# Kernel optimization log

Hardware: AMD Instinct MI355X
Metric: run time of the kernel (lower is better)

The kernel has to match this reference:

```python
import jax, jax.numpy as jnp
import numpy as np

N_HEADS = 16
N_KV_HEADS = 4
N_EMBED = 2048
HEAD_DIM = 128
SECTIONS = [16, 24, 24, 16, 24, 24]


def _process_rotary(c):
    # c: [3, B, T, HEAD_DIM] -> [B, 1, T, HEAD_DIM]
    splits = np.cumsum(SECTIONS)[:-1]
    secs = jnp.split(c, splits, axis=-1)
    out = jnp.concatenate([s[i % 3] for i, s in enumerate(secs)], axis=-1)
    return out[:, None]  # add head axis


def _rotate_half(x):
    x1, x2 = jnp.split(x, 2, axis=-1)
    return jnp.concatenate([-x2, x1], axis=-1)


def setup_inputs() -> dict:
    key = jax.random.key(0)
    ks = jax.random.split(key, 12)
    B, T = 1, 2048
    s = 0.02
    return {
        "x": jax.random.normal(ks[0], (B, T, N_EMBED), jnp.float32),
        "cos": jax.random.uniform(ks[1], (3, B, T, HEAD_DIM), jnp.float32),
        "sin": jax.random.uniform(ks[2], (3, B, T, HEAD_DIM), jnp.float32),
        "Wq": jax.random.normal(ks[3], (N_EMBED, N_EMBED), jnp.float32) * s,
        "bq": jax.random.normal(ks[4], (N_EMBED,), jnp.float32) * s,
        "Wk": jax.random.normal(ks[5], (N_EMBED, N_KV_HEADS * HEAD_DIM), jnp.float32) * s,
        "bk": jax.random.normal(ks[6], (N_KV_HEADS * HEAD_DIM,), jnp.float32) * s,
        "Wv": jax.random.normal(ks[7], (N_EMBED, N_KV_HEADS * HEAD_DIM), jnp.float32) * s,
        "bv": jax.random.normal(ks[8], (N_KV_HEADS * HEAD_DIM,), jnp.float32) * s,
        "Wo": jax.random.normal(ks[9], (N_EMBED, N_EMBED), jnp.float32) * s,
    }


def reference(x, cos, sin, Wq, bq, Wk, bk, Wv, bv, Wo):
    B, T, C = x.shape
    H, Hkv, D = N_HEADS, N_KV_HEADS, HEAD_DIM
    q = (x @ Wq + bq).reshape(B, T, H, D).transpose(0, 2, 1, 3)    # [B,H,T,D]
    k = (x @ Wk + bk).reshape(B, T, Hkv, D).transpose(0, 2, 1, 3)  # [B,Hkv,T,D]
    v = (x @ Wv + bv).reshape(B, T, Hkv, D).transpose(0, 2, 1, 3)
    # multi-section rope (cos/sin are 4-dim -> custom path)
    c = _process_rotary(cos)
    s = _process_rotary(sin)
    q = q * c + _rotate_half(q) * s
    k = k * c + _rotate_half(k) * s
    present_k, present_v = k, v
    # GQA expansion (repeat_interleave over head axis)
    r = H // Hkv
    k = jnp.repeat(k, r, axis=1)
    v = jnp.repeat(v, r, axis=1)
    # causal SDPA
    scores = jnp.einsum("bhqd,bhkd->bhqk", q, k) / jnp.sqrt(jnp.float32(D))
    causal = jnp.tril(jnp.ones((T, T), dtype=bool))
    scores = jnp.where(causal, scores, jnp.finfo(scores.dtype).min)
    attn = jax.nn.softmax(scores, axis=-1)
    y = jnp.einsum("bhqk,bhkd->bhqd", attn, v)
    y = y.transpose(0, 2, 1, 3).reshape(B, T, C)
    y = y @ Wo
    return (y, present_k, present_v)
```

## Files before the change

kernel.cpp:

```cpp
#include <hip/hip_runtime.h>

typedef unsigned short u16;
typedef __attribute__((ext_vector_type(4))) float f32x4;
typedef __attribute__((ext_vector_type(8))) __bf16 bf16x8;
typedef __attribute__((ext_vector_type(4))) u16 u16x4;


__device__ __forceinline__ u16 f2bf(float f) {
  union { float f; unsigned u; } v; v.f = f;
  unsigned r = v.u + 0x7fffu + ((v.u >> 16) & 1u);
  return (u16)(r >> 16);
}

__device__ __forceinline__ void stage16(const void* g, void* l) {
#if __has_builtin(__builtin_amdgcn_global_load_lds)
  __builtin_amdgcn_global_load_lds((const __attribute__((address_space(1))) void*)g,
                                   (__attribute__((address_space(3))) void*)l, 16, 0, 0);
#else
  *(f32x4*)l = *(const f32x4*)g;
#endif
}

__device__ __forceinline__ f32x4 mfma16(bf16x8 a, bf16x8 b, f32x4 c) {
  return __builtin_amdgcn_mfma_f32_16x16x32_bf16(a, b, c, 0, 0, 0);
}

__device__ __forceinline__ float fexp2(float x) {
#if __has_builtin(__builtin_amdgcn_exp2f)
  return __builtin_amdgcn_exp2f(x);
#else
  return exp2f(x);
#endif
}

__device__ __forceinline__ int rope_ch(int d) {
  int dd = (d < 64) ? d : d - 64;
  return (dd < 16) ? 0 : (dd < 40 ? 1 : 2);
}


__global__ void yuna_convert_bf16(const float* __restrict__ in, u16* __restrict__ out, int n4) {
  int i = blockIdx.x * blockDim.x + threadIdx.x;
  if (i < n4) {
    f32x4 v = ((const f32x4*)in)[i];
    u16x4 o;
    o.x = f2bf(v.x); o.y = f2bf(v.y); o.z = f2bf(v.z); o.w = f2bf(v.w);
    ((u16x4*)out)[i] = o;
  }
}

__global__ void yuna_transpose_bf16(const float* __restrict__ W, u16* __restrict__ out, int N) {
  __shared__ float tile[64][65];
  int k0 = blockIdx.x * 64, n0 = blockIdx.y * 64;
  int tx = threadIdx.x & 63, ty = threadIdx.x >> 6;
#pragma unroll
  for (int j = 0; j < 64; j += 4)
    tile[ty + j][tx] = W[(size_t)(k0 + ty + j) * N + n0 + tx];
  __syncthreads();
#pragma unroll
  for (int j = 0; j < 64; j += 4)
    out[(size_t)(n0 + ty + j) * 2048 + k0 + tx] = f2bf(tile[tx][ty + j]);
}

__global__ void yuna_transpose_v(const float* __restrict__ pv, u16* __restrict__ vtb) {
  __shared__ float tile[64][65];
  int t0 = blockIdx.x * 64, d0 = blockIdx.y * 64, kvh = blockIdx.z;
  int tx = threadIdx.x & 63, ty = threadIdx.x >> 6;
#pragma unroll
  for (int j = 0; j < 64; j += 4)
    tile[ty + j][tx] = pv[(size_t)(kvh * 2048 + t0 + ty + j) * 128 + d0 + tx];
  __syncthreads();
#pragma unroll
  for (int j = 0; j < 64; j += 4)
    vtb[(size_t)(kvh * 128 + d0 + ty + j) * 2048 + t0 + tx] = f2bf(tile[tx][ty + j]);
}

template <int WN>
__global__ __launch_bounds__(256, 2) void yuna_gemm_bt(
    const u16* __restrict__ A, const u16* __restrict__ Bt,
    float* __restrict__ C, int M, int N, int K) {
  constexpr int NF = WN / 16;
  constexpr int BROWS = 2 * WN;
  __shared__ __align__(16) u16 As[128 * 64];
  __shared__ __align__(16) u16 Bs[BROWS * 64];
  const int tid = threadIdx.x;
  const int wave = tid >> 6, lane = tid & 63;
  const int m0 = blockIdx.x * 128, n0 = blockIdx.y * (2 * WN);
  const int wr = (wave >> 1) * 64, wc = (wave & 1) * WN;
  const int lrow = lane & 15, lkg = lane >> 4;

  const int srow = tid >> 3;
  const int ssc = (tid & 7) ^ ((tid >> 3) & 7);
  const size_t abase = (size_t)(m0 + srow) * K + ssc * 8;
  const size_t bbase = (size_t)(n0 + srow) * K + ssc * 8;

  const f32x4 fzero = {0.f, 0.f, 0.f, 0.f};
  f32x4 acc[4][NF];
#pragma unroll
  for (int mi = 0; mi < 4; ++mi)
#pragma unroll
    for (int ni = 0; ni < NF; ++ni) acc[mi][ni] = fzero;

  const int sw = lrow & 7;
  for (int k0 = 0; k0 < K; k0 += 64) {
    __syncthreads();
#pragma unroll
    for (int it = 0; it < 4; ++it)
      stage16(A + abase + (size_t)it * 32 * K + k0, (char*)As + (tid + it * 256) * 16);
#pragma unroll
    for (int it = 0; it < BROWS / 32; ++it)
      stage16(Bt + bbase + (size_t)it * 32 * K + k0, (char*)Bs + (tid + it * 256) * 16);
    asm volatile("s_waitcnt vmcnt(0)" ::: "memory");
    __syncthreads();
#pragma unroll
    for (int kk = 0; kk < 2; ++kk) {
      const int cof = ((kk * 4 + lkg) ^ sw) << 4;
      bf16x8 af[4], bfr[NF];
#pragma unroll
      for (int mi = 0; mi < 4; ++mi)
        af[mi] = *(const bf16x8*)((const char*)As + (wr + mi * 16 + lrow) * 128 + cof);
#pragma unroll
      for (int ni = 0; ni < NF; ++ni)
        bfr[ni] = *(const bf16x8*)((const char*)Bs + (wc + ni * 16 + lrow) * 128 + cof);
#pragma unroll
      for (int mi = 0; mi < 4; ++mi)
#pragma unroll
        for (int ni = 0; ni < NF; ++ni)
          acc[mi][ni] = mfma16(af[mi], bfr[ni], acc[mi][ni]);
    }
  }
#pragma unroll
  for (int mi = 0; mi < 4; ++mi)
#pragma unroll
    for (int ni = 0; ni < NF; ++ni) {
      int r0 = m0 + wr + mi * 16 + lkg * 4;
      int c = n0 + wc + ni * 16 + lrow;
#pragma unroll
      for (int r = 0; r < 4; ++r)
        C[(size_t)(r0 + r) * N + c] = acc[mi][ni][r];
    }
}

__global__ void yuna_rope_scatter(
    const float* __restrict__ qkv, const float* __restrict__ bq,
    const float* __restrict__ bk, const float* __restrict__ bv,
    const float* __restrict__ cosp, const float* __restrict__ sinp,
    u16* __restrict__ qb, u16* __restrict__ kb,
    float* __restrict__ pk, float* __restrict__ pv) {
  const float QSCALE = 1.4426950408889634f * 0.08838834764831845f;
  int t = blockIdx.x;
  int tid = threadIdx.x;
  const float* row = qkv + (size_t)t * 3072;
  size_t cbase = (size_t)t * 128;
  for (int i = tid; i < 1024; i += 256) {
    int h = i >> 6, d = i & 63;
    float a = row[h * 128 + d] + bq[h * 128 + d];
    float b = row[h * 128 + d + 64] + bq[h * 128 + d + 64];
    float c0 = cosp[(size_t)rope_ch(d) * 262144 + cbase + d];
    float s0 = sinp[(size_t)rope_ch(d) * 262144 + cbase + d];
    float c1 = cosp[(size_t)rope_ch(d + 64) * 262144 + cbase + d + 64];
    float s1 = sinp[(size_t)rope_ch(d + 64) * 262144 + cbase + d + 64];
    float o0 = a * c0 - b * s0;
    float o1 = b * c1 + a * s1;
    size_t o = ((size_t)h * 2048 + t) * 128 + d;
    qb[o] = f2bf(o0 * QSCALE);
    qb[o + 64] = f2bf(o1 * QSCALE);
  }
  {
    int kvh = tid >> 6, d = tid & 63;
    float a = row[2048 + kvh * 128 + d] + bk[kvh * 128 + d];
    float b = row[2048 + kvh * 128 + d + 64] + bk[kvh * 128 + d + 64];
    float c0 = cosp[(size_t)rope_ch(d) * 262144 + cbase + d];
    float s0 = sinp[(size_t)rope_ch(d) * 262144 + cbase + d];
    float c1 = cosp[(size_t)rope_ch(d + 64) * 262144 + cbase + d + 64];
    float s1 = sinp[(size_t)rope_ch(d + 64) * 262144 + cbase + d + 64];
    float o0 = a * c0 - b * s0;
    float o1 = b * c1 + a * s1;
    size_t o = ((size_t)kvh * 2048 + t) * 128 + d;
    kb[o] = f2bf(o0); kb[o + 64] = f2bf(o1);
    pk[o] = o0; pk[o + 64] = o1;
  }
  for (int i = tid; i < 512; i += 256) {
    int kvh = i >> 7, d = i & 127;
    pv[((size_t)kvh * 2048 + t) * 128 + d] = row[2560 + kvh * 128 + d] + bv[kvh * 128 + d];
  }
}

__global__ __launch_bounds__(128, 2) void yuna_flash_attn(
    const u16* __restrict__ Q,
    const u16* __restrict__ Kb,
    const u16* __restrict__ Vt,
    u16* __restrict__ Y) {
  __shared__ __align__(16) u16 Ks[64 * 128];
  __shared__ __align__(16) u16 Vs[128 * 64];
  const int h = blockIdx.x;
  const int yb = blockIdx.y;
  const int qb = (yb & 1) ? (31 - (yb >> 1)) : (yb >> 1);
  const int kvh = h >> 2;
  const int tid = threadIdx.x, wave = tid >> 6, lane = tid & 63;
  const int lrow = lane & 15, lkg = lane >> 4;
  const int mloc0 = wave * 32;
  const int sw = lrow & 7;

  const int krow = tid >> 4;
  const int ksc = (tid & 15) ^ ((tid >> 4) & 7);
  const size_t kbase0 = ((size_t)(kvh * 2048 + krow) << 7) + ksc * 8;
  const int vrow = tid >> 3;
  const int vsc = (tid & 7) ^ ((tid >> 3) & 7);
  const size_t vbase0 = (size_t)(kvh * 128 + vrow) * 2048 + vsc * 8;

  bf16x8 qf[2][4];
#pragma unroll
  for (int mt = 0; mt < 2; ++mt)
#pragma unroll
    for (int kk = 0; kk < 4; ++kk)
      qf[mt][kk] = *(const bf16x8*)(Q + (((size_t)h * 2048 + qb * 64 + mloc0 + mt * 16 + lrow) << 7) + kk * 32 + lkg * 8);

  const f32x4 fzero = {0.f, 0.f, 0.f, 0.f};
  f32x4 o[8][2];
#pragma unroll
  for (int dt = 0; dt < 8; ++dt) { o[dt][0] = fzero; o[dt][1] = fzero; }
  float m_i[2] = {-1e30f, -1e30f}, l_i[2] = {0.f, 0.f};

  const int nkb = qb + 1;
  for (int kb = 0; kb < nkb; ++kb) {
    __syncthreads();
#pragma unroll
    for (int it = 0; it < 8; ++it)
      stage16(Kb + kbase0 + ((size_t)(kb * 64 + it * 8) << 7), (char*)Ks + (tid + it * 128) * 16);
#pragma unroll
    for (int it = 0; it < 8; ++it)
      stage16(Vt + vbase0 + (size_t)it * 16 * 2048 + kb * 64, (char*)Vs + (tid + it * 128) * 16);
    asm volatile("s_waitcnt vmcnt(0)" ::: "memory");
    __syncthreads();

    f32x4 s[4][2];
#pragma unroll
    for (int nt = 0; nt < 4; ++nt) { s[nt][0] = fzero; s[nt][1] = fzero; }
#pragma unroll
    for (int kk = 0; kk < 4; ++kk) {
      const int cof = ((kk * 4 + lkg) ^ sw) << 4;
      bf16x8 kf[4];
#pragma unroll
      for (int nt = 0; nt < 4; ++nt)
        kf[nt] = *(const bf16x8*)((const char*)Ks + (nt * 16 + lrow) * 256 + cof);
#pragma unroll
      for (int nt = 0; nt < 4; ++nt)
#pragma unroll
        for (int mt = 0; mt < 2; ++mt)
          s[nt][mt] = mfma16(kf[nt], qf[mt][kk], s[nt][mt]);
    }
    if (kb == qb) {
#pragma unroll
      for (int nt = 0; nt < 4; ++nt)
#pragma unroll
        for (int mt = 0; mt < 2; ++mt) {
          int m = mloc0 + mt * 16 + lrow;
#pragma unroll
          for (int r = 0; r < 4; ++r)
            if (nt * 16 + lkg * 4 + r > m) s[nt][mt][r] = -1e30f;
        }
    }
    __syncthreads();

    float alpha[2];
#pragma unroll
    for (int mt = 0; mt < 2; ++mt) {
      float mx = -1e30f;
#pragma unroll
      for (int nt = 0; nt < 4; ++nt)
#pragma unroll
        for (int r = 0; r < 4; ++r) mx = fmaxf(mx, s[nt][mt][r]);
      mx = fmaxf(mx, __shfl_xor(mx, 16));
      mx = fmaxf(mx, __shfl_xor(mx, 32));
      float mnew = fmaxf(m_i[mt], mx);
      alpha[mt] = fexp2(m_i[mt] - mnew);
      m_i[mt] = mnew;
      float ps = 0.f;
      const int m = mloc0 + mt * 16 + lrow;
      const int hh = lkg & 1;
#pragma unroll
      for (int nt = 0; nt < 4; ++nt) {
        u16x4 p4;
#pragma unroll
        for (int r = 0; r < 4; ++r) {
          float p = fexp2(s[nt][mt][r] - mnew);
          ps += p;
          p4[r] = f2bf(p);
        }
        int cc = 2 * nt + (lkg >> 1);
        *(u16x4*)((char*)Ks + m * 128 + ((cc ^ (m & 7)) << 4) + hh * 8) = p4;
      }
      ps += __shfl_xor(ps, 16);
      ps += __shfl_xor(ps, 32);
      l_i[mt] = l_i[mt] * alpha[mt] + ps;
    }
#pragma unroll
    for (int dt = 0; dt < 8; ++dt) {
      o[dt][0] *= alpha[0];
      o[dt][1] *= alpha[1];
    }

#pragma unroll
    for (int kk = 0; kk < 2; ++kk) {
      const int cof = ((kk * 4 + lkg) ^ sw) << 4;
      bf16x8 pf[2], vf[8];
#pragma unroll
      for (int mt = 0; mt < 2; ++mt) {
        int m = mloc0 + mt * 16 + lrow;
        pf[mt] = *(const bf16x8*)((const char*)Ks + m * 128 + cof);
      }
#pragma unroll
      for (int dt = 0; dt < 8; ++dt)
        vf[dt] = *(const bf16x8*)((const char*)Vs + (dt * 16 + lrow) * 128 + cof);
#pragma unroll
      for (int dt = 0; dt < 8; ++dt)
#pragma unroll
        for (int mt = 0; mt < 2; ++mt)
          o[dt][mt] = mfma16(vf[dt], pf[mt], o[dt][mt]);
    }
  }

  __syncthreads();
#pragma unroll
  for (int mt = 0; mt < 2; ++mt) {
    float inv = 1.f / l_i[mt];
    int m = mloc0 + mt * 16 + lrow;
    const int hh = lkg & 1;
#pragma unroll
    for (int dt = 0; dt < 8; ++dt) {
      u16x4 w4;
#pragma unroll
      for (int r = 0; r < 4; ++r) w4[r] = f2bf(o[dt][mt][r] * inv);
      int cc = 2 * dt + (lkg >> 1);
      *(u16x4*)((char*)Ks + m * 256 + ((cc ^ (m & 7)) << 4) + hh * 8) = w4;
    }
  }
  __syncthreads();
#pragma unroll
  for (int it = 0; it < 8; ++it) {
    int c = tid + it * 128;
    int row = c >> 4, cc = c & 15;
    f32x4 v = *(const f32x4*)((const char*)Ks + row * 256 + ((cc ^ (row & 7)) << 4));
    *(f32x4*)(Y + (size_t)(qb * 64 + row) * 2048 + h * 128 + cc * 8) = v;
  }
}


extern "C" void kernel_launch(void* const* d_in, const int* in_sizes, int n_in,
                              void* d_out, int out_size, void* d_ws, size_t ws_size,
                              hipStream_t stream) {
  const float* x = (const float*)d_in[0];
  const float* cosp = (const float*)d_in[1];
  const float* sinp = (const float*)d_in[2];
  const float* Wq = (const float*)d_in[3];
  const float* bq = (const float*)d_in[4];
  const float* Wk = (const float*)d_in[5];
  const float* bk = (const float*)d_in[6];
  const float* Wv = (const float*)d_in[7];
  const float* bv = (const float*)d_in[8];
  const float* Wo = (const float*)d_in[9];
  float* out = (float*)d_out;
  float* out_k = out + 4194304;
  float* out_v = out + 5242880;

  char* ws = (char*)d_ws;
  u16* xb   = (u16*)(ws + 0);
  u16* Wb   = (u16*)(ws + 8388608);
  u16* Wob  = (u16*)(ws + 20971520);
  float* qkv = (float*)(ws + 29360128);
  u16* qbuf = (u16*)(ws + 54525952);
  u16* kbuf = (u16*)(ws + 62914560);
  u16* vtb  = (u16*)(ws + 65011712);
  u16* yat  = (u16*)(ws + 67108864);

  yuna_convert_bf16<<<4096, 256, 0, stream>>>(x, xb, 1048576);
  yuna_transpose_bf16<<<dim3(32, 32), 256, 0, stream>>>(Wq, Wb, 2048);
  yuna_transpose_bf16<<<dim3(32, 8), 256, 0, stream>>>(Wk, Wb + (size_t)2048 * 2048, 512);
  yuna_transpose_bf16<<<dim3(32, 8), 256, 0, stream>>>(Wv, Wb + (size_t)2560 * 2048, 512);
  yuna_transpose_bf16<<<dim3(32, 32), 256, 0, stream>>>(Wo, Wob, 2048);
  yuna_gemm_bt<48><<<dim3(16, 32), 256, 0, stream>>>(xb, Wb, qkv, 2048, 3072, 2048);
  yuna_rope_scatter<<<2048, 256, 0, stream>>>(qkv, bq, bk, bv, cosp, sinp,
                                              qbuf, kbuf, out_k, out_v);
  yuna_transpose_v<<<dim3(32, 2, 4), 256, 0, stream>>>(out_v, vtb);
  yuna_flash_attn<<<dim3(16, 32), 128, 0, stream>>>(qbuf, kbuf, vtb, yat);
  yuna_gemm_bt<32><<<dim3(16, 32), 256, 0, stream>>>(yat, Wob, out, 2048, 2048, 2048);
}
```

Before: 270.4 us.

## Double-buffer K/V tiles in flash attention and merge weight transposes into one launch

The flash attention kernel now keeps two LDS buffers for K and V and prefetches the next key block while computing on the current one, waiting with partial vmcnt counts and raw s_barrier. P gets its own LDS buffer so it no longer overwrites K. The query-block ordering across blockIdx.y is changed, and the four weight transpose launches are fused into one 3D-grid launch with early exit for the smaller matrices. The larger LDS footprint may lower occupancy, and the ordering of the hand-written waitcnt and barrier calls has to be correct.

```diff
diff --git a/kernel.cpp b/kernel.cpp
--- a/kernel.cpp
+++ b/kernel.cpp
@@ -49,9 +49,20 @@
   }
 }
 
-__global__ void yuna_transpose_bf16(const float* __restrict__ W, u16* __restrict__ out, int N) {
+__global__ void yuna_prep_weights(const float* __restrict__ Wq, const float* __restrict__ Wk,
+                                  const float* __restrict__ Wv, const float* __restrict__ Wo,
+                                  u16* __restrict__ Wb, u16* __restrict__ Wob) {
   __shared__ float tile[64][65];
+  const int mat = blockIdx.z;
+  const float* W;
+  u16* out;
+  int N;
+  if (mat == 0)      { W = Wq; out = Wb;                          N = 2048; }
+  else if (mat == 1) { W = Wk; out = Wb + (size_t)2048 * 2048;    N = 512; }
+  else if (mat == 2) { W = Wv; out = Wb + (size_t)2560 * 2048;    N = 512; }
+  else               { W = Wo; out = Wob;                         N = 2048; }
   int k0 = blockIdx.x * 64, n0 = blockIdx.y * 64;
+  if (n0 >= N) return;
   int tx = threadIdx.x & 63, ty = threadIdx.x >> 6;
 #pragma unroll
   for (int j = 0; j < 64; j += 4)
@@ -191,11 +202,12 @@
     const u16* __restrict__ Kb,
     const u16* __restrict__ Vt,
     u16* __restrict__ Y) {
-  __shared__ __align__(16) u16 Ks[64 * 128];
-  __shared__ __align__(16) u16 Vs[128 * 64];
+  __shared__ __align__(16) u16 Ks[2][64 * 128];
+  __shared__ __align__(16) u16 Vs[2][128 * 64];
+  __shared__ __align__(16) u16 Ps[64 * 64];
   const int h = blockIdx.x;
   const int yb = blockIdx.y;
-  const int qb = (yb & 1) ? (31 - (yb >> 1)) : (yb >> 1);
+  const int qb = (yb < 16) ? yb : 47 - yb;
   const int kvh = h >> 2;
   const int tid = threadIdx.x, wave = tid >> 6, lane = tid & 63;
   const int lrow = lane & 15, lkg = lane >> 4;
@@ -223,16 +235,31 @@
   float m_i[2] = {-1e30f, -1e30f}, l_i[2] = {0.f, 0.f};
 
   const int nkb = qb + 1;
+
+#pragma unroll
+  for (int it = 0; it < 8; ++it)
+    stage16(Kb + kbase0 + ((size_t)(it * 8) << 7), (char*)Ks[0] + (tid + it * 128) * 16);
+#pragma unroll
+  for (int it = 0; it < 8; ++it)
+    stage16(Vt + vbase0 + (size_t)it * 16 * 2048, (char*)Vs[0] + (tid + it * 128) * 16);
+
   for (int kb = 0; kb < nkb; ++kb) {
-    __syncthreads();
-#pragma unroll
-    for (int it = 0; it < 8; ++it)
-      stage16(Kb + kbase0 + ((size_t)(kb * 64 + it * 8) << 7), (char*)Ks + (tid + it * 128) * 16);
-#pragma unroll
-    for (int it = 0; it < 8; ++it)
-      stage16(Vt + vbase0 + (size_t)it * 16 * 2048 + kb * 64, (char*)Vs + (tid + it * 128) * 16);
-    asm volatile("s_waitcnt vmcnt(0)" ::: "memory");
-    __syncthreads();
+    const int cur = kb & 1;
+    const char* Ksb = (const char*)Ks[cur];
+    const char* Vsb = (const char*)Vs[cur];
+    if (kb + 1 < nkb) {
+      char* Ksn = (char*)Ks[cur ^ 1];
+      char* Vsn = (char*)Vs[cur ^ 1];
+#pragma unroll
+      for (int it = 0; it < 8; ++it)
+        stage16(Kb + kbase0 + ((size_t)((kb + 1) * 64 + it * 8) << 7), Ksn + (tid + it * 128) * 16);
+#pragma unroll
+      for (int it = 0; it < 8; ++it)
+        stage16(Vt + vbase0 + (size_t)it * 16 * 2048 + (kb + 1) * 64, Vsn + (tid + it * 128) * 16);
+      asm volatile("s_waitcnt vmcnt(16)\n\ts_barrier" ::: "memory");
+    } else {
+      asm volatile("s_waitcnt vmcnt(0)\n\ts_barrier" ::: "memory");
+    }
 
     f32x4 s[4][2];
 #pragma unroll
@@ -243,7 +270,7 @@
       bf16x8 kf[4];
 #pragma unroll
       for (int nt = 0; nt < 4; ++nt)
-        kf[nt] = *(const bf16x8*)((const char*)Ks + (nt * 16 + lrow) * 256 + cof);
+        kf[nt] = *(const bf16x8*)(Ksb + (nt * 16 + lrow) * 256 + cof);
 #pragma unroll
       for (int nt = 0; nt < 4; ++nt)
 #pragma unroll
@@ -261,7 +288,6 @@
             if (nt * 16 + lkg * 4 + r > m) s[nt][mt][r] = -1e30f;
         }
     }
-    __syncthreads();
 
     float alpha[2];
 #pragma unroll
@@ -289,7 +315,7 @@
           p4[r] = f2bf(p);
         }
         int cc = 2 * nt + (lkg >> 1);
-        *(u16x4*)((char*)Ks + m * 128 + ((cc ^ (m & 7)) << 4) + hh * 8) = p4;
+        *(u16x4*)((char*)Ps + m * 128 + ((cc ^ (m & 7)) << 4) + hh * 8) = p4;
       }
       ps += __shfl_xor(ps, 16);
       ps += __shfl_xor(ps, 32);
@@ -308,17 +334,18 @@
 #pragma unroll
       for (int mt = 0; mt < 2; ++mt) {
         int m = mloc0 + mt * 16 + lrow;
-        pf[mt] = *(const bf16x8*)((const char*)Ks + m * 128 + cof);
+        pf[mt] = *(const bf16x8*)((char*)Ps + m * 128 + cof);
       }
 #pragma unroll
       for (int dt = 0; dt < 8; ++dt)
-        vf[dt] = *(const bf16x8*)((const char*)Vs + (dt * 16 + lrow) * 128 + cof);
+        vf[dt] = *(const bf16x8*)(Vsb + (dt * 16 + lrow) * 128 + cof);
 #pragma unroll
       for (int dt = 0; dt < 8; ++dt)
 #pragma unroll
         for (int mt = 0; mt < 2; ++mt)
           o[dt][mt] = mfma16(vf[dt], pf[mt], o[dt][mt]);
     }
+    asm volatile("s_barrier" ::: "memory");
   }
 
   __syncthreads();
@@ -333,7 +360,7 @@
 #pragma unroll
       for (int r = 0; r < 4; ++r) w4[r] = f2bf(o[dt][mt][r] * inv);
       int cc = 2 * dt + (lkg >> 1);
-      *(u16x4*)((char*)Ks + m * 256 + ((cc ^ (m & 7)) << 4) + hh * 8) = w4;
+      *(u16x4*)((char*)Ks[0] + m * 256 + ((cc ^ (m & 7)) << 4) + hh * 8) = w4;
     }
   }
   __syncthreads();
@@ -341,7 +368,7 @@
   for (int it = 0; it < 8; ++it) {
     int c = tid + it * 128;
     int row = c >> 4, cc = c & 15;
-    f32x4 v = *(const f32x4*)((const char*)Ks + row * 256 + ((cc ^ (row & 7)) << 4));
+    f32x4 v = *(const f32x4*)((const char*)Ks[0] + row * 256 + ((cc ^ (row & 7)) << 4));
     *(f32x4*)(Y + (size_t)(qb * 64 + row) * 2048 + h * 128 + cc * 8) = v;
   }
 }
@@ -375,10 +402,7 @@
   u16* yat  = (u16*)(ws + 67108864);
 
   yuna_convert_bf16<<<4096, 256, 0, stream>>>(x, xb, 1048576);
-  yuna_transpose_bf16<<<dim3(32, 32), 256, 0, stream>>>(Wq, Wb, 2048);
-  yuna_transpose_bf16<<<dim3(32, 8), 256, 0, stream>>>(Wk, Wb + (size_t)2048 * 2048, 512);
-  yuna_transpose_bf16<<<dim3(32, 8), 256, 0, stream>>>(Wv, Wb + (size_t)2560 * 2048, 512);
-  yuna_transpose_bf16<<<dim3(32, 32), 256, 0, stream>>>(Wo, Wob, 2048);
+  yuna_prep_weights<<<dim3(32, 32, 4), 256, 0, stream>>>(Wq, Wk, Wv, Wo, Wb, Wob);
   yuna_gemm_bt<48><<<dim3(16, 32), 256, 0, stream>>>(xb, Wb, qkv, 2048, 3072, 2048);
   yuna_rope_scatter<<<2048, 256, 0, stream>>>(qkv, bq, bk, bv, cosp, sinp,
                                               qbuf, kbuf, out_k, out_v);
```

After: 267.7 us. Within noise of the previous version (-1.0%).
